# Kernel tuning notes

Measured on AMD Instinct MI355X. Metric: run time of the kernel, lower is better.

Reference implementation:

```python
import jax, jax.numpy as jnp
import numpy as np

NUM_CLASSES = 21


def setup_inputs() -> dict:
    key = jax.random.key(0)
    k1, k2 = jax.random.split(key)
    B, C, H, W = 8, NUM_CLASSES, 512, 512
    inputs = jax.random.normal(k1, (B, C, H, W), dtype=jnp.float32)
    targets = jax.random.randint(k2, (B, H, W), 0, C, dtype=jnp.int64)
    return {"inputs": inputs, "targets": targets}


def reference(inputs, targets):
    # inputs: [B, C, H, W] logits; targets: [B, H, W] int labels
    B, C, H, W = inputs.shape
    # Hard predictions are detached in the original (Variable(inputs.data...))
    predicts = jax.lax.stop_gradient(jnp.argmax(inputs, axis=1))  # [B, H, W]
    probs = jax.nn.softmax(inputs, axis=1)                        # [B, C, H, W]

    classes = jnp.arange(C)
    # Per-class binary masks, vectorized over C.
    # Note: the original's i==0 branch (invert nonzero/zero) reduces to the
    # same (x == i) indicator as the i>0 branch.
    pm = predicts[:, None, :, :] == classes[None, :, None, None]  # [B, C, H, W] bool
    tm = targets[:, None, :, :] == classes[None, :, None, None]   # [B, C, H, W] bool
    union_mask = (pm | tm).astype(probs.dtype)      # union with 2 -> 1 clamp
    intersect_mask = (pm & tm).astype(probs.dtype)

    # Soft-weighted per-class sums over batch-flattened spatial dims.
    union = jnp.sum(probs * union_mask, axis=(2, 3))        # [B, C]
    intersect = jnp.sum(probs * intersect_mask, axis=(2, 3))  # [B, C]

    ratio = intersect / jnp.maximum(union, 1.0)  # [B, C]
    # Per class: MSELoss(ratio, 1) = mean over batch; then sum over classes.
    iou_loss = jnp.sum(jnp.mean((ratio - 1.0) ** 2, axis=0))
    return iou_loss
```

## Files before the change

### kernel.cpp

```cpp
#include <hip/hip_runtime.h>

#define NUM_CLASSES 21
#define HW (512 * 512)
#define BATCH 8
#define GRIDX 128
#define BLOCK 256
#define PIX_PER_BLOCK (HW / GRIDX)

#define WS_FLOATS (2 * BATCH * NUM_CLASSES)

__global__ void zero_ws_kernel(float* ws) {
    int i = blockIdx.x * blockDim.x + threadIdx.x;
    if (i < WS_FLOATS) ws[i] = 0.0f;
}

__global__ __launch_bounds__(BLOCK) void iou_partial_kernel(
        const float* __restrict__ in,
        const int* __restrict__ tgt,
        float* __restrict__ ws) {
    const int b = blockIdx.y;
    __shared__ float s_union[NUM_CLASSES];
    __shared__ float s_inter[NUM_CLASSES];
    if (threadIdx.x < NUM_CLASSES) {
        s_union[threadIdx.x] = 0.0f;
        s_inter[threadIdx.x] = 0.0f;
    }
    __syncthreads();

    const float* inb = in + (size_t)b * NUM_CLASSES * HW;
    const int*   tb  = tgt + (size_t)b * HW;
    const int start = blockIdx.x * PIX_PER_BLOCK;

    for (int p = start + threadIdx.x; p < start + PIX_PER_BLOCK; p += BLOCK) {
        const int t = tb[p];
        float v[NUM_CLASSES];
        #pragma unroll
        for (int c = 0; c < NUM_CLASSES; ++c)
            v[c] = inb[(size_t)c * HW + p];

        float m = v[0];
        int   am = 0;
        float vt = v[0];
        #pragma unroll
        for (int c = 1; c < NUM_CLASSES; ++c) {
            if (v[c] > m) { m = v[c]; am = c; }
        }
        #pragma unroll
        for (int c = 1; c < NUM_CLASSES; ++c)
            vt = (c == t) ? v[c] : vt;

        float s = 0.0f;
        #pragma unroll
        for (int c = 0; c < NUM_CLASSES; ++c)
            s += __expf(v[c] - m);
        const float inv    = 1.0f / s;
        const float p_pred = inv;
        const float p_t    = __expf(vt - m) * inv;

        atomicAdd(&s_union[am], p_pred);
        if (am == t) {
            atomicAdd(&s_inter[am], p_pred);
        } else {
            atomicAdd(&s_union[t], p_t);
        }
    }
    __syncthreads();

    if (threadIdx.x < NUM_CLASSES) {
        atomicAdd(&ws[b * NUM_CLASSES + threadIdx.x], s_union[threadIdx.x]);
        atomicAdd(&ws[BATCH * NUM_CLASSES + b * NUM_CLASSES + threadIdx.x],
                  s_inter[threadIdx.x]);
    }
}

__global__ __launch_bounds__(BLOCK) void finalize_kernel(
        const float* __restrict__ ws, float* __restrict__ out) {
    __shared__ float red[BLOCK];
    const int i = threadIdx.x;
    float val = 0.0f;
    if (i < BATCH * NUM_CLASSES) {
        const float u  = ws[i];
        const float it = ws[BATCH * NUM_CLASSES + i];
        const float ratio = it / fmaxf(u, 1.0f);
        const float d = ratio - 1.0f;
        val = d * d;
    }
    red[i] = val;
    __syncthreads();
    for (int off = BLOCK / 2; off > 0; off >>= 1) {
        if (i < off) red[i] += red[i + off];
        __syncthreads();
    }
    if (i == 0) out[0] = red[0] / (float)BATCH;
}

extern "C" void kernel_launch(void* const* d_in, const int* in_sizes, int n_in,
                              void* d_out, int out_size, void* d_ws, size_t ws_size,
                              hipStream_t stream) {
    const float* in  = (const float*)d_in[0];
    const int*   tgt = (const int*)d_in[1];
    float* ws  = (float*)d_ws;
    float* out = (float*)d_out;

    zero_ws_kernel<<<1, 512, 0, stream>>>(ws);
    dim3 grid(GRIDX, BATCH);
    iou_partial_kernel<<<grid, BLOCK, 0, stream>>>(in, tgt, ws);
    finalize_kernel<<<1, BLOCK, 0, stream>>>(ws, out);
}
```

Before: 253.3 us.

## Vectorize pixel loads to float4 and replace LDS atomics with register accumulators

Each thread now handles four pixels at a time using float4/int4 loads and computes max and sum in one online-softmax pass. Per-class union and intersection sums are kept in registers, reduced with wavefront shuffles, and only then written to shared memory with atomics. This removes the per-pixel shared-memory atomics that contended across the block and cuts the number of load instructions. In exchange it uses many more registers (two 21-entry accumulators plus four-wide state), adds extra exp calls for the online rescaling, and does 21-way select updates per pixel.

```diff
diff --git a/kernel.cpp b/kernel.cpp
--- a/kernel.cpp
+++ b/kernel.cpp
@@ -1,13 +1,14 @@
 #include <hip/hip_runtime.h>
 
-#define NUM_CLASSES 21
+#define NCLS 21
 #define HW (512 * 512)
 #define BATCH 8
 #define GRIDX 128
 #define BLOCK 256
-#define PIX_PER_BLOCK (HW / GRIDX)
+#define QUADS_PER_BLOCK ((HW / 4) / GRIDX)
+#define ITERS (QUADS_PER_BLOCK / BLOCK)
 
-#define WS_FLOATS (2 * BATCH * NUM_CLASSES)
+#define WS_FLOATS (2 * BATCH * NCLS)
 
 __global__ void zero_ws_kernel(float* ws) {
     int i = blockIdx.x * blockDim.x + threadIdx.x;
@@ -19,57 +20,86 @@
         const int* __restrict__ tgt,
         float* __restrict__ ws) {
     const int b = blockIdx.y;
-    __shared__ float s_union[NUM_CLASSES];
-    __shared__ float s_inter[NUM_CLASSES];
-    if (threadIdx.x < NUM_CLASSES) {
-        s_union[threadIdx.x] = 0.0f;
-        s_inter[threadIdx.x] = 0.0f;
-    }
-    __syncthreads();
+    const float4* __restrict__ in4 = (const float4*)(in + (size_t)b * NCLS * HW);
+    const int4*   __restrict__ tb4 = (const int4*)(tgt + (size_t)b * HW);
 
-    const float* inb = in + (size_t)b * NUM_CLASSES * HW;
-    const int*   tb  = tgt + (size_t)b * HW;
-    const int start = blockIdx.x * PIX_PER_BLOCK;
+    float u_acc[NCLS];
+    float i_acc[NCLS];
+    #pragma unroll
+    for (int c = 0; c < NCLS; ++c) { u_acc[c] = 0.0f; i_acc[c] = 0.0f; }
 
-    for (int p = start + threadIdx.x; p < start + PIX_PER_BLOCK; p += BLOCK) {
-        const int t = tb[p];
-        float v[NUM_CLASSES];
-        #pragma unroll
-        for (int c = 0; c < NUM_CLASSES; ++c)
-            v[c] = inb[(size_t)c * HW + p];
+    const int qbase = blockIdx.x * QUADS_PER_BLOCK;
 
-        float m = v[0];
-        int   am = 0;
-        float vt = v[0];
-        #pragma unroll
-        for (int c = 1; c < NUM_CLASSES; ++c) {
-            if (v[c] > m) { m = v[c]; am = c; }
+    for (int it = 0; it < ITERS; ++it) {
+        const int q = qbase + it * BLOCK + threadIdx.x;
+        const int4 tq = tb4[q];
+        const int t[4] = {tq.x, tq.y, tq.z, tq.w};
+
+        float m[4], s[4], vt[4];
+        int   am[4];
+
+        {
+            const float4 x = in4[q];
+            const float v[4] = {x.x, x.y, x.z, x.w};
+            #pragma unroll
+            for (int j = 0; j < 4; ++j) {
+                m[j] = v[j]; s[j] = 1.0f; am[j] = 0; vt[j] = v[j];
+            }
         }
         #pragma unroll
-        for (int c = 1; c < NUM_CLASSES; ++c)
-            vt = (c == t) ? v[c] : vt;
+        for (int c = 1; c < NCLS; ++c) {
+            const float4 x = in4[(size_t)c * (HW / 4) + q];
+            const float v[4] = {x.x, x.y, x.z, x.w};
+            #pragma unroll
+            for (int j = 0; j < 4; ++j) {
+                const float mn = fmaxf(m[j], v[j]);
+                s[j] = s[j] * __expf(m[j] - mn) + __expf(v[j] - mn);
+                am[j] = (v[j] > m[j]) ? c : am[j];
+                m[j] = mn;
+                vt[j] = (c == t[j]) ? v[j] : vt[j];
+            }
+        }
 
-        float s = 0.0f;
         #pragma unroll
-        for (int c = 0; c < NUM_CLASSES; ++c)
-            s += __expf(v[c] - m);
-        const float inv    = 1.0f / s;
-        const float p_pred = inv;
-        const float p_t    = __expf(vt - m) * inv;
+        for (int j = 0; j < 4; ++j) {
+            const float inv    = 1.0f / s[j];
+            const float p_pred = inv;
+            const float p_t    = __expf(vt[j] - m[j]) * inv;
+            const int   tj = t[j], aj = am[j];
+            const float w_t = (tj == aj) ? 0.0f : p_t;
+            const float ip  = (tj == aj) ? p_pred : 0.0f;
+            #pragma unroll
+            for (int c = 0; c < NCLS; ++c) {
+                u_acc[c] += ((c == aj) ? p_pred : 0.0f) + ((c == tj) ? w_t : 0.0f);
+                i_acc[c] += (c == aj) ? ip : 0.0f;
+            }
+        }
+    }
 
-        atomicAdd(&s_union[am], p_pred);
-        if (am == t) {
-            atomicAdd(&s_inter[am], p_pred);
-        } else {
-            atomicAdd(&s_union[t], p_t);
+    #pragma unroll
+    for (int c = 0; c < NCLS; ++c) {
+        #pragma unroll
+        for (int off = 32; off > 0; off >>= 1) {
+            u_acc[c] += __shfl_down(u_acc[c], off, 64);
+            i_acc[c] += __shfl_down(i_acc[c], off, 64);
+        }
+    }
+
+    __shared__ float s_u[NCLS];
+    __shared__ float s_i[NCLS];
+    if (threadIdx.x < NCLS) { s_u[threadIdx.x] = 0.0f; s_i[threadIdx.x] = 0.0f; }
+    __syncthreads();
+    if ((threadIdx.x & 63) == 0) {
+        #pragma unroll
+        for (int c = 0; c < NCLS; ++c) {
+            atomicAdd(&s_u[c], u_acc[c]);
+            atomicAdd(&s_i[c], i_acc[c]);
         }
     }
     __syncthreads();
-
-    if (threadIdx.x < NUM_CLASSES) {
-        atomicAdd(&ws[b * NUM_CLASSES + threadIdx.x], s_union[threadIdx.x]);
-        atomicAdd(&ws[BATCH * NUM_CLASSES + b * NUM_CLASSES + threadIdx.x],
-                  s_inter[threadIdx.x]);
+    if (threadIdx.x < NCLS) {
+        atomicAdd(&ws[b * NCLS + threadIdx.x], s_u[threadIdx.x]);
+        atomicAdd(&ws[BATCH * NCLS + b * NCLS + threadIdx.x], s_i[threadIdx.x]);
     }
 }
 
@@ -78,9 +108,9 @@
     __shared__ float red[BLOCK];
     const int i = threadIdx.x;
     float val = 0.0f;
-    if (i < BATCH * NUM_CLASSES) {
+    if (i < BATCH * NCLS) {
         const float u  = ws[i];
-        const float it = ws[BATCH * NUM_CLASSES + i];
+        const float it = ws[BATCH * NCLS + i];
         const float ratio = it / fmaxf(u, 1.0f);
         const float d = ratio - 1.0f;
         val = d * d;
```

Result: no change. 256.5 us (+1.2%).
